# Kernel optimization log

Measured on AMD Instinct MI355X. Metric: run time of the kernel, lower is better.

Reference implementation:

```python
import jax, jax.numpy as jnp
from jax import lax
import numpy as np

B, C, T = 16, 128, 16384
MIDC, GROUPS, PATCH = 128, 4, 8
DROP_RATE = 0.1
NEG_BIG = -1e9


def setup_inputs() -> dict:
    key = jax.random.key(0)
    ks = jax.random.split(key, 9)
    wordnum = T // PATCH
    x = jax.random.normal(ks[0], (B, C, T), jnp.float32)
    condition = jax.random.normal(ks[1], (B, C, T), jnp.float32)
    # torch.bernoulli(k, dropRate) * -1e9 : Bernoulli(p=0.1) mask, shape of k
    mask = jax.random.bernoulli(ks[2], DROP_RATE, (B, MIDC, wordnum, PATCH)).astype(jnp.float32) * NEG_BIG
    wQ = jax.random.normal(ks[3], (MIDC, C // GROUPS, 5, 1), jnp.float32) * 0.05
    bQ = jax.random.normal(ks[4], (MIDC,), jnp.float32) * 0.05
    wKV = jax.random.normal(ks[5], (2 * MIDC, C // GROUPS, 5, 1), jnp.float32) * 0.05
    bKV = jax.random.normal(ks[6], (2 * MIDC,), jnp.float32) * 0.05
    wOut = jax.random.normal(ks[7], (C, MIDC, 3), jnp.float32) * 0.05
    bOut = jax.random.normal(ks[8], (C,), jnp.float32) * 0.05
    return {"x": x, "condition": condition, "mask": mask, "wQ": wQ, "bQ": bQ,
            "wKV": wKV, "bKV": bKV, "wOut": wOut, "bOut": bOut,
            "patch": PATCH, "groups": GROUPS}


def _conv2d_same(x, w, b, groups):
    # kernel (5,1), padding 'same' -> (2,2) on H, (0,0) on W
    y = lax.conv_general_dilated(x, w, (1, 1), [(2, 2), (0, 0)],
                                 dimension_numbers=('NCHW', 'OIHW', 'NCHW'),
                                 feature_group_count=groups)
    return y + b[None, :, None, None]


def _conv1d_same(x, w, b):
    # kernel 3, padding 'same' -> (1,1)
    y = lax.conv_general_dilated(x, w, (1,), [(1, 1)],
                                 dimension_numbers=('NCH', 'OIH', 'NCH'))
    return y + b[None, :, None]


def reference(x, condition, mask, wQ, bQ, wKV, bKV, wOut, bOut, patch, groups):
    b, c, t = x.shape
    pad_x = (-t) % patch
    pad_c = (-condition.shape[-1]) % patch
    x = jnp.pad(x, ((0, 0), (0, 0), (0, pad_x)))
    condition = jnp.pad(condition, ((0, 0), (0, 0), (0, pad_c)))
    wordnum = x.shape[-1] // patch
    x4 = x.reshape(b, c, wordnum, patch)
    c4 = condition.reshape(b, c, condition.shape[-1] // patch, patch)

    q = _conv2d_same(c4, wQ, bQ, groups)              # [B, midC, W, P]
    kv = _conv2d_same(x4, wKV, bKV, groups)           # [B, 2*midC, W, P]
    k, v = jnp.split(kv, 2, axis=1)
    k = k + lax.stop_gradient(mask)

    midc = q.shape[1]
    cp = midc * patch
    # [B, midC, W, P] -> [B, W, midC*P]
    q = q.transpose(0, 2, 1, 3).reshape(b, wordnum, cp)
    k = k.transpose(0, 2, 1, 3).reshape(b, wordnum, cp)
    v = v.transpose(0, 2, 1, 3).reshape(b, wordnum, cp)

    q = jax.nn.softmax(q, axis=-1)   # over feature dim
    k = jax.nn.softmax(k, axis=-2)   # over wordNum dim

    kv_mat = jnp.einsum('Bki,Bkj->Bij', k, v)   # [B, CP, CP]
    out = jnp.einsum('Bik,Bkj->Bij', q, kv_mat)  # [B, W, CP]

    out = out.reshape(b, wordnum, midc, patch).transpose(0, 2, 1, 3).reshape(b, midc, wordnum * patch)
    out = _conv1d_same(out, wOut, bOut)          # [B, C, W*P]
    if pad_x != 0:
        out = out[:, :, :-pad_x]
    return out
```

## Files before the change

kernel.cpp:

```cpp
#include <hip/hip_runtime.h>
#include <stdint.h>

#define B_    16
#define C_    128
#define T_    16384
#define W_    2048
#define CP_   1024

typedef unsigned short u16;
typedef __attribute__((ext_vector_type(4))) unsigned short u16x4;
typedef __attribute__((ext_vector_type(8))) unsigned short u16x8;
typedef __attribute__((ext_vector_type(8))) short bf16x8;
typedef __attribute__((ext_vector_type(4))) float f32x4;

#define OFF_Q     0ull
#define OFF_KT    67108864ull
#define OFF_ATT   67108864ull
#define OFF_VT    134234112ull
#define OFF_KVT   201342976ull
#define OFF_W2    234897408ull
#define WS_NEEDED 234995712ull

__device__ __forceinline__ u16 f2bf(float f) {
  union { float f; uint32_t u; } v; v.f = f;
  return (u16)((v.u + 0x7FFFu + ((v.u >> 16) & 1u)) >> 16);
}
__device__ __forceinline__ float bf2f(u16 h) {
  union { uint32_t u; float f; } v; v.u = ((uint32_t)h) << 16;
  return v.f;
}
__device__ __forceinline__ void gload16(const void* g, void* l) {
  __builtin_amdgcn_global_load_lds(
      (const __attribute__((address_space(1))) uint32_t*)g,
      (__attribute__((address_space(3))) uint32_t*)l, 16, 0, 0);
}
__device__ __forceinline__ float wred_max(float v) {
  #pragma unroll
  for (int o = 32; o; o >>= 1) v = fmaxf(v, __shfl_xor(v, o));
  return v;
}
__device__ __forceinline__ float wred_sum(float v) {
  #pragma unroll
  for (int o = 32; o; o >>= 1) v += __shfl_xor(v, o);
  return v;
}

__global__ __launch_bounds__(256) void conv_q_kernel(
    const float* __restrict__ cond, const float* __restrict__ wQ,
    const float* __restrict__ bQ, u16* __restrict__ qout)
{
  __shared__ __align__(16) float sIn[128 * 96];
  const int b = blockIdx.y, w0 = blockIdx.x * 8;
  const float* cb = cond + (size_t)b * C_ * T_;
  const int tlo = w0 * 8 - 16;
  for (int f = threadIdx.x; f < 3072; f += 256) {
    int ch = f / 24;
    int off = (f % 24) * 4;
    int t = tlo + off;
    float4 val;
    if (t >= 0 && t <= T_ - 4) {
      val = *(const float4*)(cb + (size_t)ch * T_ + t);
    } else {
      float tmp[4];
      #pragma unroll
      for (int e = 0; e < 4; e++) { int tt = t + e; tmp[e] = (tt >= 0 && tt < T_) ? cb[(size_t)ch * T_ + tt] : 0.f; }
      val = make_float4(tmp[0], tmp[1], tmp[2], tmp[3]);
    }
    *(float4*)&sIn[ch * 96 + off] = val;
  }
  __syncthreads();

  const int m = threadIdx.x & 127, p0 = (threadIdx.x >> 7) * 4;
  const int g = m >> 5;
  float acc[8][4];
  #pragma unroll
  for (int w = 0; w < 8; w++) { acc[w][0] = acc[w][1] = acc[w][2] = acc[w][3] = 0.f; }
  const float* wm = wQ + (size_t)m * 160;
  const float* sg = sIn + g * 32 * 96 + p0;
  for (int ic = 0; ic < 32; ic++) {
    float w5[5];
    #pragma unroll
    for (int d = 0; d < 5; d++) w5[d] = wm[ic * 5 + d];
    const float* srow = sg + ic * 96;
    float4 vv[12];
    #pragma unroll
    for (int ww = 0; ww < 12; ww++) vv[ww] = *(const float4*)(srow + ww * 8);
    #pragma unroll
    for (int d = 0; d < 5; d++) {
      #pragma unroll
      for (int w = 0; w < 8; w++) {
        float4 x = vv[w + d];
        acc[w][0] += w5[d] * x.x; acc[w][1] += w5[d] * x.y;
        acc[w][2] += w5[d] * x.z; acc[w][3] += w5[d] * x.w;
      }
    }
  }
  const float bias = bQ[m];
  #pragma unroll
  for (int w = 0; w < 8; w++) {
    u16x4 o;
    #pragma unroll
    for (int e = 0; e < 4; e++) o[e] = f2bf(acc[w][e] + bias);
    *(u16x4*)(qout + ((size_t)(b * W_ + w0 + w) * CP_ + m * 8 + p0)) = o;
  }
}

__global__ __launch_bounds__(512) void conv_kv_kernel(
    const float* __restrict__ x, const float* __restrict__ wKV,
    const float* __restrict__ bKV, const float* __restrict__ mask,
    u16* __restrict__ kT, u16* __restrict__ vT)
{
  __shared__ __align__(16) float sIn[128 * 96];
  const int b = blockIdx.y, w0 = blockIdx.x * 8;
  const float* xb = x + (size_t)b * C_ * T_;
  const int tlo = w0 * 8 - 16;
  for (int f = threadIdx.x; f < 3072; f += 512) {
    int ch = f / 24;
    int off = (f % 24) * 4;
    int t = tlo + off;
    float4 val;
    if (t >= 0 && t <= T_ - 4) {
      val = *(const float4*)(xb + (size_t)ch * T_ + t);
    } else {
      float tmp[4];
      #pragma unroll
      for (int e = 0; e < 4; e++) { int tt = t + e; tmp[e] = (tt >= 0 && tt < T_) ? xb[(size_t)ch * T_ + tt] : 0.f; }
      val = make_float4(tmp[0], tmp[1], tmp[2], tmp[3]);
    }
    *(float4*)&sIn[ch * 96 + off] = val;
  }
  __syncthreads();

  const int oc = threadIdx.x >> 1, p0 = (threadIdx.x & 1) * 4;
  const int g = oc >> 6;
  float acc[8][4];
  #pragma unroll
  for (int w = 0; w < 8; w++) { acc[w][0] = acc[w][1] = acc[w][2] = acc[w][3] = 0.f; }
  const float* wm = wKV + (size_t)oc * 160;
  const float* sg = sIn + g * 32 * 96 + p0;
  for (int ic = 0; ic < 32; ic++) {
    float w5[5];
    #pragma unroll
    for (int d = 0; d < 5; d++) w5[d] = wm[ic * 5 + d];
    const float* srow = sg + ic * 96;
    float4 vv[12];
    #pragma unroll
    for (int ww = 0; ww < 12; ww++) vv[ww] = *(const float4*)(srow + ww * 8);
    #pragma unroll
    for (int d = 0; d < 5; d++) {
      #pragma unroll
      for (int w = 0; w < 8; w++) {
        float4 xv = vv[w + d];
        acc[w][0] += w5[d] * xv.x; acc[w][1] += w5[d] * xv.y;
        acc[w][2] += w5[d] * xv.z; acc[w][3] += w5[d] * xv.w;
      }
    }
  }
  const float bias = bKV[oc];
  if (oc < 128) {
    const float* mb = mask + (((size_t)(b * 128 + oc)) * W_ + w0) * 8 + p0;
    float mv[8][4];
    #pragma unroll
    for (int w = 0; w < 8; w++) {
      float4 t4 = *(const float4*)(mb + w * 8);
      mv[w][0] = t4.x; mv[w][1] = t4.y; mv[w][2] = t4.z; mv[w][3] = t4.w;
    }
    #pragma unroll
    for (int pp = 0; pp < 4; pp++) {
      u16x8 o;
      #pragma unroll
      for (int w = 0; w < 8; w++) o[w] = f2bf(acc[w][pp] + bias + mv[w][pp]);
      *(u16x8*)(kT + ((size_t)(b * CP_ + oc * 8 + p0 + pp)) * W_ + w0) = o;
    }
  } else {
    const int j = (oc - 128) * 8;
    #pragma unroll
    for (int pp = 0; pp < 4; pp++) {
      u16x8 o;
      #pragma unroll
      for (int w = 0; w < 8; w++) o[w] = f2bf(acc[w][pp] + bias);
      *(u16x8*)(vT + ((size_t)(b * CP_ + j + p0 + pp)) * W_ + w0) = o;
    }
  }
}

__global__ __launch_bounds__(256) void softmax_q_kernel(u16* __restrict__ q)
{
  __shared__ float red[4];
  u16* p = q + (size_t)blockIdx.x * CP_ + threadIdx.x * 4;
  u16x4 raw = *(const u16x4*)p;
  float xv[4];
  #pragma unroll
  for (int e = 0; e < 4; e++) xv[e] = bf2f(raw[e]);
  float mx = fmaxf(fmaxf(xv[0], xv[1]), fmaxf(xv[2], xv[3]));
  mx = wred_max(mx);
  if ((threadIdx.x & 63) == 0) red[threadIdx.x >> 6] = mx;
  __syncthreads();
  mx = fmaxf(fmaxf(red[0], red[1]), fmaxf(red[2], red[3]));
  __syncthreads();
  float ev[4], s = 0.f;
  #pragma unroll
  for (int e = 0; e < 4; e++) { ev[e] = __expf(xv[e] - mx); s += ev[e]; }
  s = wred_sum(s);
  if ((threadIdx.x & 63) == 0) red[threadIdx.x >> 6] = s;
  __syncthreads();
  s = red[0] + red[1] + red[2] + red[3];
  float inv = 1.f / s;
  u16x4 o;
  #pragma unroll
  for (int e = 0; e < 4; e++) o[e] = f2bf(ev[e] * inv);
  *(u16x4*)p = o;
}

__global__ __launch_bounds__(256) void softmax_k_kernel(u16* __restrict__ kT)
{
  __shared__ float red[4];
  u16* p = kT + (size_t)blockIdx.x * W_ + threadIdx.x * 8;
  u16x8 raw = *(const u16x8*)p;
  float xv[8];
  #pragma unroll
  for (int e = 0; e < 8; e++) xv[e] = bf2f(raw[e]);
  float mx = -3.4e38f;
  #pragma unroll
  for (int e = 0; e < 8; e++) mx = fmaxf(mx, xv[e]);
  mx = wred_max(mx);
  if ((threadIdx.x & 63) == 0) red[threadIdx.x >> 6] = mx;
  __syncthreads();
  mx = fmaxf(fmaxf(red[0], red[1]), fmaxf(red[2], red[3]));
  __syncthreads();
  float ev[8], s = 0.f;
  #pragma unroll
  for (int e = 0; e < 8; e++) { ev[e] = __expf(xv[e] - mx); s += ev[e]; }
  s = wred_sum(s);
  if ((threadIdx.x & 63) == 0) red[threadIdx.x >> 6] = s;
  __syncthreads();
  s = red[0] + red[1] + red[2] + red[3];
  float inv = 1.f / s;
  u16x8 o;
  #pragma unroll
  for (int e = 0; e < 8; e++) o[e] = f2bf(ev[e] * inv);
  *(u16x8*)p = o;
}

__global__ __launch_bounds__(256) void prep_kernel(
    const float* __restrict__ wOut, u16* __restrict__ w2)
{
  int idx = blockIdx.x * 256 + threadIdx.x;
  if (idx < 3 * 128 * 128) {
    int dt = idx >> 14, c = (idx >> 7) & 127, m = idx & 127;
    w2[idx] = f2bf(wOut[((size_t)c * 128 + m) * 3 + dt]);
  }
}

__global__ __launch_bounds__(256) void zero_pad_kernel(u16* __restrict__ attnT)
{
  int idx = blockIdx.x * 256 + threadIdx.x;
  int b = idx >> 8, r = (idx >> 7) & 1, m = idx & 127;
  attnT[((size_t)b * (T_ + 2) + (r ? (T_ + 1) : 0)) * 128 + m] = 0;
}

template<int MODE>
__global__ __launch_bounds__(256) void gemm_bt_kernel(
    const u16* __restrict__ A, const u16* __restrict__ Bt, u16* __restrict__ out,
    int M, int N, int K)
{
  __shared__ __align__(16) u16 ldsA[4096];
  __shared__ __align__(16) u16 ldsB[4096];
  const int b = blockIdx.z;
  const int i0 = blockIdx.x * 128, j0 = blockIdx.y * 128;
  const int tid = threadIdx.x, lane = tid & 63, wv = tid >> 6;
  const int wr = wv >> 1, wc = wv & 1;
  const u16* Ab = A + (size_t)b * M * K + (size_t)i0 * K;
  const u16* Bb = Bt + (size_t)b * N * K + (size_t)j0 * K;

  const int srow0 = wv * 32 + (lane >> 2);
  const int sslot = lane & 3;
  const int frow = lane & 15, fkq = lane >> 4;

  f32x4 acc[4][4];
  #pragma unroll
  for (int m = 0; m < 4; m++)
    #pragma unroll
    for (int n = 0; n < 4; n++) acc[m][n] = (f32x4)0.f;

  for (int kt = 0; kt < K; kt += 32) {
    #pragma unroll
    for (int q = 0; q < 2; q++) {
      int row = srow0 + q * 16;
      int gslot = sslot ^ ((row >> 1) & 3);
      gload16(Ab + (size_t)row * K + kt + gslot * 8, &ldsA[row * 32 + sslot * 8]);
      gload16(Bb + (size_t)row * K + kt + gslot * 8, &ldsB[row * 32 + sslot * 8]);
    }
    __syncthreads();
    bf16x8 af[4], bf[4];
    #pragma unroll
    for (int m = 0; m < 4; m++) {
      int row = wr * 64 + m * 16 + frow;
      af[m] = *(const bf16x8*)&ldsA[row * 32 + (fkq ^ ((row >> 1) & 3)) * 8];
    }
    #pragma unroll
    for (int n = 0; n < 4; n++) {
      int row = wc * 64 + n * 16 + frow;
      bf[n] = *(const bf16x8*)&ldsB[row * 32 + (fkq ^ ((row >> 1) & 3)) * 8];
    }
    #pragma unroll
    for (int m = 0; m < 4; m++)
      #pragma unroll
      for (int n = 0; n < 4; n++)
        acc[m][n] = __builtin_amdgcn_mfma_f32_16x16x32_bf16(af[m], bf[n], acc[m][n], 0, 0, 0);
    __syncthreads();
  }

  const int rb = (lane >> 4) * 4, cl = lane & 15;
  #pragma unroll
  for (int m = 0; m < 4; m++) {
    #pragma unroll
    for (int n = 0; n < 4; n++) {
      #pragma unroll
      for (int r = 0; r < 4; r++) {
        int gr = i0 + wr * 64 + m * 16 + rb + r;
        int gc = j0 + wc * 64 + n * 16 + cl;
        u16 v = f2bf(acc[m][n][r]);
        if (MODE == 0) {
          out[((size_t)b * M + gr) * N + gc] = v;
        } else {
          out[((size_t)b * (T_ + 2) + 1 + (size_t)gr * 8 + (gc & 7)) * 128 + (gc >> 3)] = v;
        }
      }
    }
  }
}

__global__ __launch_bounds__(256) void convout_kernel(
    const u16* __restrict__ w2, const u16* __restrict__ attnT,
    const float* __restrict__ bOut, float* __restrict__ out)
{
  __shared__ __align__(16) u16 ldsA[4096];
  __shared__ __align__(16) u16 ldsB[4096];
  const int b = blockIdx.z;
  const int t0 = blockIdx.y * 128;
  const int tid = threadIdx.x, lane = tid & 63, wv = tid >> 6;
  const int wr = wv >> 1, wc = wv & 1;
  const u16* Bb = attnT + (size_t)b * (T_ + 2) * 128;

  const int srow0 = wv * 32 + (lane >> 2);
  const int sslot = lane & 3;
  const int frow = lane & 15, fkq = lane >> 4;

  f32x4 acc[4][4];
  #pragma unroll
  for (int m = 0; m < 4; m++)
    #pragma unroll
    for (int n = 0; n < 4; n++) acc[m][n] = (f32x4)0.f;

  for (int s = 0; s < 12; s++) {
    int dt = s >> 2, kk = (s & 3) * 32;
    #pragma unroll
    for (int q = 0; q < 2; q++) {
      int row = srow0 + q * 16;
      int gslot = sslot ^ ((row >> 1) & 3);
      gload16(w2 + (size_t)dt * 16384 + (size_t)row * 128 + kk + gslot * 8,
              &ldsA[row * 32 + sslot * 8]);
      gload16(Bb + (size_t)(t0 + row + dt) * 128 + kk + gslot * 8,
              &ldsB[row * 32 + sslot * 8]);
    }
    __syncthreads();
    bf16x8 af[4], bf[4];
    #pragma unroll
    for (int m = 0; m < 4; m++) {
      int row = wr * 64 + m * 16 + frow;
      af[m] = *(const bf16x8*)&ldsA[row * 32 + (fkq ^ ((row >> 1) & 3)) * 8];
    }
    #pragma unroll
    for (int n = 0; n < 4; n++) {
      int row = wc * 64 + n * 16 + frow;
      bf[n] = *(const bf16x8*)&ldsB[row * 32 + (fkq ^ ((row >> 1) & 3)) * 8];
    }
    #pragma unroll
    for (int m = 0; m < 4; m++)
      #pragma unroll
      for (int n = 0; n < 4; n++)
        acc[m][n] = __builtin_amdgcn_mfma_f32_16x16x32_bf16(af[m], bf[n], acc[m][n], 0, 0, 0);
    __syncthreads();
  }

  const int rb = (lane >> 4) * 4, cl = lane & 15;
  #pragma unroll
  for (int m = 0; m < 4; m++) {
    #pragma unroll
    for (int n = 0; n < 4; n++) {
      #pragma unroll
      for (int r = 0; r < 4; r++) {
        int c = wr * 64 + m * 16 + rb + r;
        int t = t0 + wc * 64 + n * 16 + cl;
        out[((size_t)b * 128 + c) * T_ + t] = acc[m][n][r] + bOut[c];
      }
    }
  }
}

extern "C" void kernel_launch(void* const* d_in, const int* in_sizes, int n_in,
                              void* d_out, int out_size, void* d_ws, size_t ws_size,
                              hipStream_t stream)
{
  const float* x    = (const float*)d_in[0];
  const float* cond = (const float*)d_in[1];
  const float* mask = (const float*)d_in[2];
  const float* wQ   = (const float*)d_in[3];
  const float* bQ   = (const float*)d_in[4];
  const float* wKV  = (const float*)d_in[5];
  const float* bKV  = (const float*)d_in[6];
  const float* wOut = (const float*)d_in[7];
  const float* bOut = (const float*)d_in[8];
  float* out = (float*)d_out;

  if (ws_size < WS_NEEDED) return;

  char* ws = (char*)d_ws;
  u16* q     = (u16*)(ws + OFF_Q);
  u16* kT    = (u16*)(ws + OFF_KT);
  u16* attnT = (u16*)(ws + OFF_ATT);
  u16* vT    = (u16*)(ws + OFF_VT);
  u16* kvT   = (u16*)(ws + OFF_KVT);
  u16* w2    = (u16*)(ws + OFF_W2);

  conv_q_kernel<<<dim3(256, 16), dim3(256), 0, stream>>>(cond, wQ, bQ, q);
  conv_kv_kernel<<<dim3(256, 16), dim3(512), 0, stream>>>(x, wKV, bKV, mask, kT, vT);
  prep_kernel<<<dim3(192), dim3(256), 0, stream>>>(wOut, w2);
  softmax_q_kernel<<<dim3(32768), dim3(256), 0, stream>>>(q);
  softmax_k_kernel<<<dim3(16384), dim3(256), 0, stream>>>(kT);
  gemm_bt_kernel<0><<<dim3(8, 8, 16), dim3(256), 0, stream>>>(vT, kT, kvT, 1024, 1024, 2048);
  zero_pad_kernel<<<dim3(16), dim3(256), 0, stream>>>(attnT);
  gemm_bt_kernel<1><<<dim3(16, 8, 16), dim3(256), 0, stream>>>(q, kvT, attnT, 2048, 1024, 1024);
  convout_kernel<<<dim3(1, 128, 16), dim3(256), 0, stream>>>(w2, attnT, bOut, out);
}
```

Measured before the change: 1.258 ms.

## Recast grouped Q/KV convolutions as bf16x3 split MFMA GEMMs

```diff
diff --git a/kernel.cpp b/kernel.cpp
--- a/kernel.cpp
+++ b/kernel.cpp
@@ -19,7 +19,11 @@
 #define OFF_VT    134234112ull
 #define OFF_KVT   201342976ull
 #define OFF_W2    234897408ull
-#define WS_NEEDED 234995712ull
+#define OFF_WQH   234995712ull
+#define OFF_WQL   235036672ull
+#define OFF_WKH   235077632ull
+#define OFF_WKL   235159552ull
+#define WS_NEEDED 235241472ull
 
 __device__ __forceinline__ u16 f2bf(float f) {
   union { float f; uint32_t u; } v; v.f = f;
@@ -28,6 +32,12 @@
 __device__ __forceinline__ float bf2f(u16 h) {
   union { uint32_t u; float f; } v; v.u = ((uint32_t)h) << 16;
   return v.f;
+}
+__device__ __forceinline__ void split2(float v, u16& h, u16& l) {
+  union { float f; uint32_t u; } c; c.f = v;
+  h = (u16)(c.u >> 16);
+  union { uint32_t u; float f; } hf; hf.u = c.u & 0xFFFF0000u;
+  l = f2bf(v - hf.f);
 }
 __device__ __forceinline__ void gload16(const void* g, void* l) {
   __builtin_amdgcn_global_load_lds(
@@ -45,142 +55,189 @@
   return v;
 }
 
-__global__ __launch_bounds__(256) void conv_q_kernel(
-    const float* __restrict__ cond, const float* __restrict__ wQ,
-    const float* __restrict__ bQ, u16* __restrict__ qout)
-{
-  __shared__ __align__(16) float sIn[128 * 96];
-  const int b = blockIdx.y, w0 = blockIdx.x * 8;
-  const float* cb = cond + (size_t)b * C_ * T_;
-  const int tlo = w0 * 8 - 16;
-  for (int f = threadIdx.x; f < 3072; f += 256) {
-    int ch = f / 24;
-    int off = (f % 24) * 4;
-    int t = tlo + off;
-    float4 val;
-    if (t >= 0 && t <= T_ - 4) {
-      val = *(const float4*)(cb + (size_t)ch * T_ + t);
-    } else {
-      float tmp[4];
-      #pragma unroll
-      for (int e = 0; e < 4; e++) { int tt = t + e; tmp[e] = (tt >= 0 && tt < T_) ? cb[(size_t)ch * T_ + tt] : 0.f; }
-      val = make_float4(tmp[0], tmp[1], tmp[2], tmp[3]);
-    }
-    *(float4*)&sIn[ch * 96 + off] = val;
-  }
-  __syncthreads();
-
-  const int m = threadIdx.x & 127, p0 = (threadIdx.x >> 7) * 4;
-  const int g = m >> 5;
-  float acc[8][4];
-  #pragma unroll
-  for (int w = 0; w < 8; w++) { acc[w][0] = acc[w][1] = acc[w][2] = acc[w][3] = 0.f; }
-  const float* wm = wQ + (size_t)m * 160;
-  const float* sg = sIn + g * 32 * 96 + p0;
-  for (int ic = 0; ic < 32; ic++) {
-    float w5[5];
-    #pragma unroll
-    for (int d = 0; d < 5; d++) w5[d] = wm[ic * 5 + d];
-    const float* srow = sg + ic * 96;
-    float4 vv[12];
-    #pragma unroll
-    for (int ww = 0; ww < 12; ww++) vv[ww] = *(const float4*)(srow + ww * 8);
-    #pragma unroll
-    for (int d = 0; d < 5; d++) {
-      #pragma unroll
-      for (int w = 0; w < 8; w++) {
-        float4 x = vv[w + d];
-        acc[w][0] += w5[d] * x.x; acc[w][1] += w5[d] * x.y;
-        acc[w][2] += w5[d] * x.z; acc[w][3] += w5[d] * x.w;
+#define TP 160
+#define KP 168
+
+template<int MODE>
+__global__ __launch_bounds__(256) void conv_mfma_kernel(
+    const float* __restrict__ in, const u16* __restrict__ wh,
+    const u16* __restrict__ wl, const float* __restrict__ bias,
+    const float* __restrict__ mask, u16* __restrict__ outA, u16* __restrict__ outV)
+{
+  __shared__ __align__(16) u16 lds[31744];
+  u16* Sh = lds;
+  u16* Sl = lds + 5120;
+  u16* Bt = lds + 10240;
+
+  const int tid = threadIdx.x, lane = tid & 63, wv = tid >> 6;
+  const int t0 = blockIdx.x * 128;
+  const int chunk = blockIdx.y;
+  const int b = blockIdx.z;
+  const int g = (MODE == 0) ? chunk : (chunk >> 1);
+  const int oc0 = chunk * 32;
+  const float* in_b = in + ((size_t)b * C_ + g * 32) * T_;
+
+  const int wr = wv >> 1, wc = wv & 1;
+  const int frow = lane & 15, fkq = lane >> 4;
+
+  bf16x8 ah[5], al[5];
+  {
+    const u16* hp = wh + (size_t)(oc0 + wr * 16 + frow) * 160 + fkq * 8;
+    const u16* lp = wl + (size_t)(oc0 + wr * 16 + frow) * 160 + fkq * 8;
+    #pragma unroll
+    for (int s = 0; s < 5; s++) {
+      ah[s] = *(const bf16x8*)(hp + s * 32);
+      al[s] = *(const bf16x8*)(lp + s * 32);
+    }
+  }
+
+  {
+    #pragma unroll
+    for (int it = 0; it < 5; it++) {
+      int v = tid + it * 256;
+      int row = v / 40;
+      int off = (v % 40) * 4;
+      int gt = t0 - 16 + off;
+      float4 val;
+      if (gt >= 0 && gt + 3 < T_) {
+        val = *(const float4*)(in_b + (size_t)row * T_ + gt);
+      } else {
+        float tmp[4];
+        #pragma unroll
+        for (int e = 0; e < 4; e++) {
+          int tt = gt + e;
+          tmp[e] = (tt >= 0 && tt < T_) ? in_b[(size_t)row * T_ + tt] : 0.f;
+        }
+        val = make_float4(tmp[0], tmp[1], tmp[2], tmp[3]);
       }
-    }
-  }
-  const float bias = bQ[m];
-  #pragma unroll
-  for (int w = 0; w < 8; w++) {
-    u16x4 o;
-    #pragma unroll
-    for (int e = 0; e < 4; e++) o[e] = f2bf(acc[w][e] + bias);
-    *(u16x4*)(qout + ((size_t)(b * W_ + w0 + w) * CP_ + m * 8 + p0)) = o;
-  }
-}
-
-__global__ __launch_bounds__(512) void conv_kv_kernel(
-    const float* __restrict__ x, const float* __restrict__ wKV,
-    const float* __restrict__ bKV, const float* __restrict__ mask,
-    u16* __restrict__ kT, u16* __restrict__ vT)
-{
-  __shared__ __align__(16) float sIn[128 * 96];
-  const int b = blockIdx.y, w0 = blockIdx.x * 8;
-  const float* xb = x + (size_t)b * C_ * T_;
-  const int tlo = w0 * 8 - 16;
-  for (int f = threadIdx.x; f < 3072; f += 512) {
-    int ch = f / 24;
-    int off = (f % 24) * 4;
-    int t = tlo + off;
-    float4 val;
-    if (t >= 0 && t <= T_ - 4) {
-      val = *(const float4*)(xb + (size_t)ch * T_ + t);
-    } else {
-      float tmp[4];
-      #pragma unroll
-      for (int e = 0; e < 4; e++) { int tt = t + e; tmp[e] = (tt >= 0 && tt < T_) ? xb[(size_t)ch * T_ + tt] : 0.f; }
-      val = make_float4(tmp[0], tmp[1], tmp[2], tmp[3]);
-    }
-    *(float4*)&sIn[ch * 96 + off] = val;
-  }
-  __syncthreads();
-
-  const int oc = threadIdx.x >> 1, p0 = (threadIdx.x & 1) * 4;
-  const int g = oc >> 6;
-  float acc[8][4];
-  #pragma unroll
-  for (int w = 0; w < 8; w++) { acc[w][0] = acc[w][1] = acc[w][2] = acc[w][3] = 0.f; }
-  const float* wm = wKV + (size_t)oc * 160;
-  const float* sg = sIn + g * 32 * 96 + p0;
-  for (int ic = 0; ic < 32; ic++) {
-    float w5[5];
-    #pragma unroll
-    for (int d = 0; d < 5; d++) w5[d] = wm[ic * 5 + d];
-    const float* srow = sg + ic * 96;
-    float4 vv[12];
-    #pragma unroll
-    for (int ww = 0; ww < 12; ww++) vv[ww] = *(const float4*)(srow + ww * 8);
-    #pragma unroll
-    for (int d = 0; d < 5; d++) {
-      #pragma unroll
-      for (int w = 0; w < 8; w++) {
-        float4 xv = vv[w + d];
-        acc[w][0] += w5[d] * xv.x; acc[w][1] += w5[d] * xv.y;
-        acc[w][2] += w5[d] * xv.z; acc[w][3] += w5[d] * xv.w;
+      float vf[4] = {val.x, val.y, val.z, val.w};
+      u16x4 h4, l4;
+      #pragma unroll
+      for (int e = 0; e < 4; e++) {
+        u16 hs, ls;
+        split2(vf[e], hs, ls);
+        h4[e] = hs;
+        l4[e] = ls;
       }
-    }
-  }
-  const float bias = bKV[oc];
-  if (oc < 128) {
-    const float* mb = mask + (((size_t)(b * 128 + oc)) * W_ + w0) * 8 + p0;
-    float mv[8][4];
-    #pragma unroll
-    for (int w = 0; w < 8; w++) {
-      float4 t4 = *(const float4*)(mb + w * 8);
-      mv[w][0] = t4.x; mv[w][1] = t4.y; mv[w][2] = t4.z; mv[w][3] = t4.w;
-    }
-    #pragma unroll
-    for (int pp = 0; pp < 4; pp++) {
-      u16x8 o;
-      #pragma unroll
-      for (int w = 0; w < 8; w++) o[w] = f2bf(acc[w][pp] + bias + mv[w][pp]);
-      *(u16x8*)(kT + ((size_t)(b * CP_ + oc * 8 + p0 + pp)) * W_ + w0) = o;
+      *(u16x4*)&Sh[row * TP + off] = h4;
+      *(u16x4*)&Sl[row * TP + off] = l4;
+    }
+  }
+  __syncthreads();
+
+  {
+    const int t = tid & 127, kg0 = tid >> 7;
+    #pragma unroll
+    for (int i = 0; i < 10; i++) {
+      int kg = kg0 + i * 2;
+      int d = kg >> 2, ic0 = (kg & 3) * 8;
+      int sb = t + d * 8;
+      u16x8 vv;
+      #pragma unroll
+      for (int e = 0; e < 8; e++) vv[e] = Sh[(ic0 + e) * TP + sb];
+      *(u16x8*)&Bt[t * KP + kg * 8] = vv;
+    }
+  }
+  __syncthreads();
+
+  f32x4 acc[4];
+  #pragma unroll
+  for (int n = 0; n < 4; n++) acc[n] = (f32x4)0.f;
+  #pragma unroll
+  for (int s = 0; s < 5; s++) {
+    #pragma unroll
+    for (int n = 0; n < 4; n++) {
+      bf16x8 bb = *(const bf16x8*)&Bt[(wc * 64 + n * 16 + frow) * KP + s * 32 + fkq * 8];
+      acc[n] = __builtin_amdgcn_mfma_f32_16x16x32_bf16(ah[s], bb, acc[n], 0, 0, 0);
+      acc[n] = __builtin_amdgcn_mfma_f32_16x16x32_bf16(al[s], bb, acc[n], 0, 0, 0);
+    }
+  }
+  __syncthreads();
+
+  {
+    const int t = tid & 127, kg0 = tid >> 7;
+    #pragma unroll
+    for (int i = 0; i < 10; i++) {
+      int kg = kg0 + i * 2;
+      int d = kg >> 2, ic0 = (kg & 3) * 8;
+      int sb = t + d * 8;
+      u16x8 vv;
+      #pragma unroll
+      for (int e = 0; e < 8; e++) vv[e] = Sl[(ic0 + e) * TP + sb];
+      *(u16x8*)&Bt[t * KP + kg * 8] = vv;
+    }
+  }
+  __syncthreads();
+
+  #pragma unroll
+  for (int s = 0; s < 5; s++) {
+    #pragma unroll
+    for (int n = 0; n < 4; n++) {
+      bf16x8 bb = *(const bf16x8*)&Bt[(wc * 64 + n * 16 + frow) * KP + s * 32 + fkq * 8];
+      acc[n] = __builtin_amdgcn_mfma_f32_16x16x32_bf16(ah[s], bb, acc[n], 0, 0, 0);
+    }
+  }
+
+  const int rb = (lane >> 4) * 4, cl = lane & 15;
+  float bv[4];
+  #pragma unroll
+  for (int r = 0; r < 4; r++) bv[r] = bias[oc0 + wr * 16 + rb + r];
+  if (MODE == 1 && chunk < 4) {
+    #pragma unroll
+    for (int n = 0; n < 4; n++) {
+      int tcol = t0 + wc * 64 + n * 16 + cl;
+      #pragma unroll
+      for (int r = 0; r < 4; r++) {
+        float mv = mask[((size_t)(b * 128 + oc0 + wr * 16 + rb + r)) * 16384 + tcol];
+        acc[n][r] += bv[r] + mv;
+      }
     }
   } else {
-    const int j = (oc - 128) * 8;
-    #pragma unroll
-    for (int pp = 0; pp < 4; pp++) {
-      u16x8 o;
-      #pragma unroll
-      for (int w = 0; w < 8; w++) o[w] = f2bf(acc[w][pp] + bias);
-      *(u16x8*)(vT + ((size_t)(b * CP_ + j + p0 + pp)) * W_ + w0) = o;
-    }
+    #pragma unroll
+    for (int n = 0; n < 4; n++)
+      #pragma unroll
+      for (int r = 0; r < 4; r++) acc[n][r] += bv[r];
+  }
+  __syncthreads();
+
+  if (MODE == 0) {
+    u16* stg = Bt;
+    #pragma unroll
+    for (int n = 0; n < 4; n++) {
+      int col = wc * 64 + n * 16 + cl;
+      int wl_ = col >> 3, p = col & 7;
+      #pragma unroll
+      for (int r = 0; r < 4; r++)
+        stg[wl_ * 264 + (wr * 16 + rb + r) * 8 + p] = f2bf(acc[n][r]);
+    }
+    __syncthreads();
+    int wl_ = tid >> 4, seg = (tid & 15) * 16;
+    u16x8 o0 = *(u16x8*)&stg[wl_ * 264 + seg];
+    u16x8 o1 = *(u16x8*)&stg[wl_ * 264 + seg + 8];
+    size_t ob = ((size_t)b * W_ + (t0 >> 3) + wl_) * CP_ + g * 256 + seg;
+    *(u16x8*)&outA[ob] = o0;
+    *(u16x8*)&outA[ob + 8] = o1;
+  } else {
+    u16* stg = Bt;
+    #pragma unroll
+    for (int n = 0; n < 4; n++) {
+      int col = wc * 64 + n * 16 + cl;
+      int wl_ = col >> 3, p = col & 7;
+      #pragma unroll
+      for (int r = 0; r < 4; r++)
+        stg[(wr * 16 + rb + r) * 136 + p * 16 + wl_] = f2bf(acc[n][r]);
+    }
+    __syncthreads();
+    int ocl = tid >> 3, p = tid & 7;
+    u16x8 o0 = *(u16x8*)&stg[ocl * 136 + p * 16];
+    u16x8 o1 = *(u16x8*)&stg[ocl * 136 + p * 16 + 8];
+    int w0 = t0 >> 3;
+    u16* dst;
+    size_t rowg;
+    if (chunk < 4) { dst = outA; rowg = (size_t)b * CP_ + (oc0 + ocl) * 8 + p; }
+    else           { dst = outV; rowg = (size_t)b * CP_ + (oc0 - 128 + ocl) * 8 + p; }
+    *(u16x8*)&dst[rowg * W_ + w0] = o0;
+    *(u16x8*)&dst[rowg * W_ + w0 + 8] = o1;
   }
 }
 
@@ -243,12 +300,27 @@
 }
 
 __global__ __launch_bounds__(256) void prep_kernel(
-    const float* __restrict__ wOut, u16* __restrict__ w2)
+    const float* __restrict__ wQ, const float* __restrict__ wKV,
+    const float* __restrict__ wOut, u16* __restrict__ w2,
+    u16* __restrict__ qh, u16* __restrict__ ql,
+    u16* __restrict__ kvh, u16* __restrict__ kvl)
 {
   int idx = blockIdx.x * 256 + threadIdx.x;
   if (idx < 3 * 128 * 128) {
     int dt = idx >> 14, c = (idx >> 7) & 127, m = idx & 127;
     w2[idx] = f2bf(wOut[((size_t)c * 128 + m) * 3 + dt]);
+  }
+  if (idx < 61440) {
+    const float* src; u16 *dh, *dl; int oc;
+    int k = idx % 160;
+    if (idx < 20480) { oc = idx / 160; src = wQ;  dh = qh;  dl = ql; }
+    else             { oc = (idx - 20480) / 160; src = wKV; dh = kvh; dl = kvl; }
+    int d = k >> 5, ic = k & 31;
+    float w = src[(size_t)oc * 160 + ic * 5 + d];
+    u16 h, l;
+    split2(w, h, l);
+    dh[(size_t)oc * 160 + k] = h;
+    dl[(size_t)oc * 160 + k] = l;
   }
 }
 
@@ -423,10 +495,14 @@
   u16* vT    = (u16*)(ws + OFF_VT);
   u16* kvT   = (u16*)(ws + OFF_KVT);
   u16* w2    = (u16*)(ws + OFF_W2);
-
-  conv_q_kernel<<<dim3(256, 16), dim3(256), 0, stream>>>(cond, wQ, bQ, q);
-  conv_kv_kernel<<<dim3(256, 16), dim3(512), 0, stream>>>(x, wKV, bKV, mask, kT, vT);
-  prep_kernel<<<dim3(192), dim3(256), 0, stream>>>(wOut, w2);
+  u16* wQh   = (u16*)(ws + OFF_WQH);
+  u16* wQl   = (u16*)(ws + OFF_WQL);
+  u16* wKVh  = (u16*)(ws + OFF_WKH);
+  u16* wKVl  = (u16*)(ws + OFF_WKL);
+
+  prep_kernel<<<dim3(240), dim3(256), 0, stream>>>(wQ, wKV, wOut, w2, wQh, wQl, wKVh, wKVl);
+  conv_mfma_kernel<0><<<dim3(128, 4, 16), dim3(256), 0, stream>>>(cond, wQh, wQl, bQ, nullptr, q, nullptr);
+  conv_mfma_kernel<1><<<dim3(128, 8, 16), dim3(256), 0, stream>>>(x, wKVh, wKVl, bKV, mask, kT, vT);
   softmax_q_kernel<<<dim3(32768), dim3(256), 0, stream>>>(q);
   softmax_k_kernel<<<dim3(16384), dim3(256), 0, stream>>>(kT);
   gemm_bt_kernel<0><<<dim3(8, 8, 16), dim3(256), 0, stream>>>(vT, kT, kvT, 1024, 1024, 2048);
```

After: 1.090 ms. 1.15x faster.
